# Kernel optimization log

Measured on AMD Instinct MI355X. Metric: run time of the kernel, lower is better.

The kernel has to match this reference:

```python
import jax, jax.numpy as jnp
import numpy as np

NEGPOS_RATIO = 3


def _smooth_l1(pred, tgt):
    d = jnp.abs(pred - tgt)
    return jnp.where(d < 1.0, 0.5 * d * d, d - 0.5)


def setup_inputs() -> dict:
    key = jax.random.key(0)
    B, P, C = 64, 8732, 81
    ks = jax.random.split(key, 7)
    loc_dataT = jax.random.normal(ks[0], (B, P, 4), jnp.float32)
    conf_dataT = jax.random.normal(ks[1], (B, P, C), jnp.float32)
    loc_dataS = jax.random.normal(ks[2], (B, P, 4), jnp.float32)
    conf_dataS = jax.random.normal(ks[3], (B, P, C), jnp.float32)
    loc_t = jax.random.normal(ks[4], (B, P, 4), jnp.float32)
    is_pos = jax.random.uniform(ks[5], (B, P)) < 0.02
    labels = jax.random.randint(ks[6], (B, P), 1, C, dtype=jnp.int32)
    conf_t = jnp.where(is_pos, labels, 0).astype(jnp.int32)
    return {
        "loc_dataT": loc_dataT, "conf_dataT": conf_dataT,
        "loc_dataS": loc_dataS, "conf_dataS": conf_dataS,
        "loc_t": loc_t, "conf_t": conf_t,
    }


def _multibox_losses(loc_dataT, conf_dataT, loc_dataS, conf_dataS, loc_t, conf_t):
    B, P, C = conf_dataT.shape
    pos = conf_t > 0                                    # [B,P]
    posf = pos.astype(conf_dataT.dtype)

    # Localization SmoothL1 over positive priors (reduction='sum')
    loss_lT = jnp.sum(_smooth_l1(loc_dataT, loc_t) * posf[..., None])
    loss_lS = jnp.sum(_smooth_l1(loc_dataS, loc_t) * posf[..., None])

    # Per-prior CE loss: logsumexp(conf) - conf[gt]  (== -log_softmax[gt])
    def per_prior_ce(conf):
        lse = jax.nn.logsumexp(conf, axis=-1)           # [B,P]
        gt = jnp.take_along_axis(conf, conf_t[..., None].astype(jnp.int32), axis=-1)[..., 0]
        return lse - gt

    lcT = per_prior_ce(conf_dataT)                      # [B,P]
    lcS = per_prior_ce(conf_dataS)

    # Hard negative mining: rank negatives by loss (positives zeroed first)
    def neg_mask(lc, num_neg):
        lc_m = jnp.where(pos, 0.0, lc)
        order = jnp.argsort(-lc_m, axis=1)              # descending sort indices
        rank = jnp.argsort(order, axis=1)               # rank of each prior
        return rank < num_neg

    num_pos = jnp.sum(pos.astype(jnp.int32), axis=1, keepdims=True)   # [B,1]
    num_neg = jnp.minimum(NEGPOS_RATIO * num_pos, P - 1)
    negT = neg_mask(lcT, num_neg)
    negS = neg_mask(lcS, num_neg)

    # Confidence CE over positives + mined negatives (reduction='sum')
    loss_cT = jnp.sum(jnp.where(pos | negT, lcT, 0.0))
    loss_cS = jnp.sum(jnp.where(pos | negS, lcS, 0.0))

    N = jnp.sum(num_pos).astype(conf_dataT.dtype)
    return jnp.stack([loss_lT / N, loss_cT / N, loss_lS / N, loss_cS / N])


def reference(loc_dataT, conf_dataT, loc_dataS, conf_dataS, loc_t, conf_t):
    # Teacher branch is detached in the original module.
    loc_dataT = jax.lax.stop_gradient(loc_dataT)
    conf_dataT = jax.lax.stop_gradient(conf_dataT)
    return _multibox_losses(loc_dataT, conf_dataT, loc_dataS, conf_dataS, loc_t, conf_t)
```

## Files before the change

kernel.cpp:

```cpp
#include <hip/hip_runtime.h>

#define BB 64
#define PP 8732
#define CC 81
#define RPW 16
#define WSLOTS ((RPW * CC) / 4)
#define WSTRIDE (WSLOTS + RPW)
#define WPB 4
#define ROWS_PB (RPW * WPB)


__device__ __forceinline__ float sl1(float d) {
    d = fabsf(d);
    return d < 1.0f ? 0.5f * d * d : d - 0.5f;
}

__device__ __forceinline__ float blockReduceF(float v, volatile float* sb) {
    for (int off = 32; off; off >>= 1) v += __shfl_xor(v, off, 64);
    __syncthreads();
    if ((threadIdx.x & 63) == 0) sb[threadIdx.x >> 6] = v;
    __syncthreads();
    float r = 0.0f;
    int nw = blockDim.x >> 6;
    for (int i = 0; i < nw; ++i) r += sb[i];
    return r;
}

__device__ __forceinline__ int blockReduceI(int v, volatile int* sb) {
    for (int off = 32; off; off >>= 1) v += __shfl_xor(v, off, 64);
    __syncthreads();
    if ((threadIdx.x & 63) == 0) sb[threadIdx.x >> 6] = v;
    __syncthreads();
    int r = 0;
    int nw = blockDim.x >> 6;
    for (int i = 0; i < nw; ++i) r += sb[i];
    return r;
}

__global__ void kInit(float* acc, int* numpos, int* ctr, float* locPart) {
    int t = threadIdx.x;
    if (t < 4) acc[t] = 0.0f;
    if (t < BB) { numpos[t] = 0; locPart[t] = 0.0f; locPart[BB + t] = 0.0f; }
    if (t == 0) ctr[0] = 0;
}

__device__ __forceinline__ void processSlot(int i, float4 v,
                                            float* psum, float* spill) {
    int f = i << 2;
    int r0 = f / 81;
    int rem = f - r0 * 81;
    float e0 = __expf(v.x), e1 = __expf(v.y), e2 = __expf(v.z), e3 = __expf(v.w);
    float t01 = e0 + e1;
    float tot = t01 + e2 + e3;
    float ps = tot;
    if (rem >= 78) {
        int ns = 81 - rem;
        float a = (ns == 1) ? e0 : ((ns == 2) ? t01 : t01 + e2);
        ps = a;
        spill[r0 + 1] = tot - a;
    }
    psum[i] = ps;
}

__global__ __launch_bounds__(256, 8) void kStream(
        const float* __restrict__ confT, const float* __restrict__ confS,
        const int* __restrict__ conft,
        const float4* __restrict__ locT4, const float4* __restrict__ locS4,
        const float4* __restrict__ loct4,
        float* __restrict__ lcT, float* __restrict__ lcS,
        float* __restrict__ locPart, int* __restrict__ numpos) {
    __shared__ float lds[WPB * WSTRIDE];
    int b = blockIdx.y;
    int z = blockIdx.z;
    int tid = threadIdx.x;
    int w = tid >> 6, lane = tid & 63;
    int row0 = blockIdx.x * ROWS_PB + w * RPW;
    int nr = min(RPW, PP - row0);
    const float* __restrict__ conf = z ? confS : confT;
    float* __restrict__ dst = z ? lcS : lcT;
    float* psum = lds + w * WSTRIDE;
    float* spill = psum + WSLOTS;

    float sT = 0.0f, sS = 0.0f;
    int cnt = 0;
    int g_ = 0;

    if (nr > 0) {
        size_t rowBase = (size_t)b * PP + row0;
        const float* __restrict__ rowp = conf + rowBase * (size_t)CC;
        const float4* __restrict__ g4 = (const float4*)rowp;
        bool hasrow = lane < nr;
        if (hasrow) g_ = conft[rowBase + lane];
        float gtv = 0.0f;

        if (nr == RPW) {
            float4 v0 = g4[lane];
            float4 v1 = g4[lane + 64];
            float4 v2 = g4[lane + 128];
            float4 v3 = g4[lane + 192];
            float4 v4 = g4[lane + 256];
            float4 vx;
            bool extra = lane < (WSLOTS - 320);
            if (extra) vx = g4[320 + lane];
            if (hasrow) gtv = rowp[lane * CC + g_];
            processSlot(lane,       v0, psum, spill);
            processSlot(lane + 64,  v1, psum, spill);
            processSlot(lane + 128, v2, psum, spill);
            processSlot(lane + 192, v3, psum, spill);
            processSlot(lane + 256, v4, psum, spill);
            if (extra) processSlot(320 + lane, vx, psum, spill);
        } else {
            int nq = (nr * CC) >> 2;
            for (int i = lane; i < nq; i += 64)
                processSlot(i, g4[i], psum, spill);
            if (hasrow) gtv = rowp[lane * CC + g_];
        }

        if (z == 0 && hasrow && g_ > 0) {
            size_t idx = rowBase + lane;
            float4 gt = loct4[idx];
            float4 aT = locT4[idx];
            float4 aS = locS4[idx];
            sT = sl1(aT.x - gt.x) + sl1(aT.y - gt.y) + sl1(aT.z - gt.z) + sl1(aT.w - gt.w);
            sS = sl1(aS.x - gt.x) + sl1(aS.y - gt.y) + sl1(aS.z - gt.z) + sl1(aS.w - gt.w);
            cnt = 1;
        }

        asm volatile("s_waitcnt lgkmcnt(0)" ::: "memory");
        __builtin_amdgcn_sched_barrier(0);

        int r = lane >> 2, h = lane & 3;
        float gv = __shfl(gtv, r, 64);
        int   gr = __shfl(g_,  r, 64);
        if (r < nr) {
            int i0 = (81 * r + 3) >> 2;
            int i1 = (81 * (r + 1) + 3) >> 2;
            float s = (h == 0 && (r & 3)) ? spill[r] : 0.0f;
            for (int i = i0 + h; i < i1; i += 4) s += psum[i];
            s += __shfl_xor(s, 1, 64);
            s += __shfl_xor(s, 2, 64);
            if (h == 0) {
                float lc = __logf(s) - gv;
                dst[rowBase + r] = (gr > 0) ? -(lc + 1.0f) : lc;
            }
        }
    }

    if (z == 0) {
        for (int off = 32; off; off >>= 1) {
            sT  += __shfl_xor(sT,  off, 64);
            sS  += __shfl_xor(sS,  off, 64);
            cnt += __shfl_xor(cnt, off, 64);
        }
        if (lane == 0 && cnt) {
            atomicAdd(&locPart[b], sT);
            atomicAdd(&locPart[BB + b], sS);
            atomicAdd(&numpos[b], cnt);
        }
    }
}

__global__ __launch_bounds__(1024) void kC(const float* __restrict__ lcT,
                                           const float* __restrict__ lcS,
                                           const int* __restrict__ numpos,
                                           const float* __restrict__ locPart,
                                           float* acc, int* ctr,
                                           float* __restrict__ out) {
    __shared__ unsigned keys[PP];
    __shared__ int whist[16 * 256];
    __shared__ int hist[256];
    __shared__ float fsb[16];
    __shared__ int isb[16];
    __shared__ int selBin, selAbove, lastFlag, wsum[4];
    int b = blockIdx.y;
    int tid = threadIdx.x;
    int lane = tid & 63;
    const float* src = ((blockIdx.x == 0) ? lcT : lcS) + (size_t)b * PP;

    float posSum = 0.0f;
    for (int i = tid; i < PP; i += 1024) {
        float v = src[i];
        keys[i] = (v < 0.0f) ? 0u : __float_as_uint(v);
        if (v < 0.0f) posSum += (-v - 1.0f);
    }
    posSum = blockReduceF(posSum, fsb);

    int np = numpos[b];
    int k = min(3 * np, PP - 1);
    float mined = 0.0f;
    if (k > 0) {
        unsigned prefix = 0;
        int kk = k;
        int wid = tid >> 6;
        for (int round = 0; round < 4; ++round) {
            int shift = 24 - 8 * round;
            for (int i = tid; i < 16 * 256; i += 1024) whist[i] = 0;
            __syncthreads();
            for (int i = tid; i < PP; i += 1024) {
                unsigned key = keys[i];
                bool match = (round == 0) || ((key >> (shift + 8)) == prefix);
                if (match) atomicAdd(&whist[(wid << 8) | ((key >> shift) & 0xFF)], 1);
            }
            __syncthreads();
            if (tid < 256) {
                int h2 = 0;
                #pragma unroll
                for (int w = 0; w < 16; ++w) h2 += whist[(w << 8) | tid];
                hist[tid] = h2;
            }
            __syncthreads();
            int x = (tid < 256) ? hist[tid] : 0;
            for (int d = 1; d < 64; d <<= 1) {
                int y = __shfl_down(x, d, 64);
                if (lane + d < 64) x += y;
            }
            if (tid < 256 && lane == 0) wsum[tid >> 6] = x;
            __syncthreads();
            if (tid < 256) {
                int wv = tid >> 6;
                int add = 0;
                if (wv < 3) add += wsum[wv + 1];
                if (wv < 2) add += wsum[wv + 2];
                if (wv < 1) add += wsum[wv + 3];
                int sfx = x + add;
                hist[tid] = sfx;
            }
            __syncthreads();
            if (tid < 256) {
                int above = (tid < 255) ? hist[tid + 1] : 0;
                if (above < kk && hist[tid] >= kk) {
                    selBin = tid;
                    selAbove = above;
                }
            }
            __syncthreads();
            prefix = (prefix << 8) | (unsigned)selBin;
            kk -= selAbove;
            __syncthreads();
        }
        int c = 0;
        float s = 0.0f;
        for (int i = tid; i < PP; i += 1024) {
            unsigned key = keys[i];
            if (key > prefix) { c += 1; s += __uint_as_float(key); }
        }
        c = blockReduceI(c, isb);
        s = blockReduceF(s, fsb);
        mined = s + (float)(k - c) * __uint_as_float(prefix);
    }
    if (tid == 0) {
        atomicAdd(&acc[(blockIdx.x == 0) ? 2 : 3], posSum + mined);
        __threadfence();
        int old = atomicAdd(ctr, 1);
        lastFlag = (old == 2 * BB - 1) ? 1 : 0;
    }
    __syncthreads();
    if (lastFlag) {
        __threadfence();
        int v = 0;
        float pT = 0.0f, pS = 0.0f;
        if (tid < BB) {
            v  = __hip_atomic_load(&numpos[tid], __ATOMIC_RELAXED, __HIP_MEMORY_SCOPE_AGENT);
            pT = __hip_atomic_load(&locPart[tid], __ATOMIC_RELAXED, __HIP_MEMORY_SCOPE_AGENT);
            pS = __hip_atomic_load(&locPart[BB + tid], __ATOMIC_RELAXED, __HIP_MEMORY_SCOPE_AGENT);
        }
        if (tid < 64) {
            for (int off = 32; off; off >>= 1) {
                v  += __shfl_xor(v,  off, 64);
                pT += __shfl_xor(pT, off, 64);
                pS += __shfl_xor(pS, off, 64);
            }
        }
        if (tid == 0) {
            float N = (float)v;
            float a2 = __hip_atomic_load(&acc[2], __ATOMIC_RELAXED, __HIP_MEMORY_SCOPE_AGENT);
            float a3 = __hip_atomic_load(&acc[3], __ATOMIC_RELAXED, __HIP_MEMORY_SCOPE_AGENT);
            out[0] = pT / N;
            out[1] = a2 / N;
            out[2] = pS / N;
            out[3] = a3 / N;
        }
    }
}

extern "C" void kernel_launch(void* const* d_in, const int* in_sizes, int n_in,
                              void* d_out, int out_size, void* d_ws, size_t ws_size,
                              hipStream_t stream) {
    const float* locT  = (const float*)d_in[0];
    const float* confT = (const float*)d_in[1];
    const float* locS  = (const float*)d_in[2];
    const float* confS = (const float*)d_in[3];
    const float* loct  = (const float*)d_in[4];
    const int*   conft = (const int*)d_in[5];
    float* out = (float*)d_out;

    float* lcT = (float*)d_ws;
    float* lcS = lcT + (size_t)BB * PP;
    float* acc = lcS + (size_t)BB * PP;
    int* numpos = (int*)(acc + 4);
    int* ctr = numpos + BB;
    float* locPart = (float*)(ctr + 1);

    kInit<<<1, 64, 0, stream>>>(acc, numpos, ctr, locPart);

    dim3 gS((PP + ROWS_PB - 1) / ROWS_PB, BB, 2);
    kStream<<<gS, 256, 0, stream>>>(confT, confS, conft,
                                    (const float4*)locT, (const float4*)locS,
                                    (const float4*)loct, lcT, lcS,
                                    locPart, numpos);

    dim3 gC(2, BB);
    kC<<<gC, 1024, 0, stream>>>(lcT, lcS, numpos, locPart, acc, ctr, out);
}
```

Measured before the change: 425.4 us.

## Process teacher and student conf rows in the same wave instead of separate grid z

The kernel drops the z grid dimension. Each wave now loads both the teacher and student conf tiles up front, then runs the exp/partial-sum and per-row reduction twice, reusing the same LDS scratch. The goal is to double the memory-level parallelism per wave, share the conft label load, and halve the block count. In exchange, register pressure rises, which the lower launch bound of 6 waves per SIMD accommodates, and occupancy may drop.

```diff
diff --git a/kernel.cpp b/kernel.cpp
--- a/kernel.cpp
+++ b/kernel.cpp
@@ -62,7 +62,29 @@
     psum[i] = ps;
 }
 
-__global__ __launch_bounds__(256, 8) void kStream(
+__device__ __forceinline__ void waveReduceStore(float* __restrict__ dst,
+                                                size_t rowBase, int nr, int lane,
+                                                const float* psum,
+                                                const float* spill,
+                                                float gtv, int g_) {
+    int r = lane >> 2, h = lane & 3;
+    float gv = __shfl(gtv, r, 64);
+    int   gr = __shfl(g_,  r, 64);
+    if (r < nr) {
+        int i0 = (81 * r + 3) >> 2;
+        int i1 = (81 * (r + 1) + 3) >> 2;
+        float s = (h == 0 && (r & 3)) ? spill[r] : 0.0f;
+        for (int i = i0 + h; i < i1; i += 4) s += psum[i];
+        s += __shfl_xor(s, 1, 64);
+        s += __shfl_xor(s, 2, 64);
+        if (h == 0) {
+            float lc = __logf(s) - gv;
+            dst[rowBase + r] = (gr > 0) ? -(lc + 1.0f) : lc;
+        }
+    }
+}
+
+__global__ __launch_bounds__(256, 6) void kStream(
         const float* __restrict__ confT, const float* __restrict__ confS,
         const int* __restrict__ conft,
         const float4* __restrict__ locT4, const float4* __restrict__ locS4,
@@ -71,52 +93,87 @@
         float* __restrict__ locPart, int* __restrict__ numpos) {
     __shared__ float lds[WPB * WSTRIDE];
     int b = blockIdx.y;
-    int z = blockIdx.z;
     int tid = threadIdx.x;
     int w = tid >> 6, lane = tid & 63;
     int row0 = blockIdx.x * ROWS_PB + w * RPW;
     int nr = min(RPW, PP - row0);
-    const float* __restrict__ conf = z ? confS : confT;
-    float* __restrict__ dst = z ? lcS : lcT;
     float* psum = lds + w * WSTRIDE;
     float* spill = psum + WSLOTS;
 
     float sT = 0.0f, sS = 0.0f;
     int cnt = 0;
     int g_ = 0;
+    bool hasrow = false;
 
     if (nr > 0) {
         size_t rowBase = (size_t)b * PP + row0;
-        const float* __restrict__ rowp = conf + rowBase * (size_t)CC;
-        const float4* __restrict__ g4 = (const float4*)rowp;
-        bool hasrow = lane < nr;
-        if (hasrow) g_ = conft[rowBase + lane];
-        float gtv = 0.0f;
+        const float* __restrict__ rowT = confT + rowBase * (size_t)CC;
+        const float* __restrict__ rowS = confS + rowBase * (size_t)CC;
+        const float4* __restrict__ gT4 = (const float4*)rowT;
+        const float4* __restrict__ gS4 = (const float4*)rowS;
+        hasrow = lane < nr;
 
         if (nr == RPW) {
-            float4 v0 = g4[lane];
-            float4 v1 = g4[lane + 64];
-            float4 v2 = g4[lane + 128];
-            float4 v3 = g4[lane + 192];
-            float4 v4 = g4[lane + 256];
-            float4 vx;
+            if (hasrow) g_ = conft[rowBase + lane];
+            float4 t0 = gT4[lane];
+            float4 t1 = gT4[lane + 64];
+            float4 t2 = gT4[lane + 128];
+            float4 t3 = gT4[lane + 192];
+            float4 t4 = gT4[lane + 256];
+            float4 tx;
             bool extra = lane < (WSLOTS - 320);
-            if (extra) vx = g4[320 + lane];
-            if (hasrow) gtv = rowp[lane * CC + g_];
-            processSlot(lane,       v0, psum, spill);
-            processSlot(lane + 64,  v1, psum, spill);
-            processSlot(lane + 128, v2, psum, spill);
-            processSlot(lane + 192, v3, psum, spill);
-            processSlot(lane + 256, v4, psum, spill);
-            if (extra) processSlot(320 + lane, vx, psum, spill);
+            if (extra) tx = gT4[320 + lane];
+            float4 s0 = gS4[lane];
+            float4 s1 = gS4[lane + 64];
+            float4 s2 = gS4[lane + 128];
+            float4 s3 = gS4[lane + 192];
+            float4 s4 = gS4[lane + 256];
+            float4 sx;
+            if (extra) sx = gS4[320 + lane];
+            float gtvT = 0.0f, gtvS = 0.0f;
+            if (hasrow) {
+                gtvT = rowT[lane * CC + g_];
+                gtvS = rowS[lane * CC + g_];
+            }
+            __builtin_amdgcn_sched_barrier(0);
+
+            processSlot(lane,       t0, psum, spill);
+            processSlot(lane + 64,  t1, psum, spill);
+            processSlot(lane + 128, t2, psum, spill);
+            processSlot(lane + 192, t3, psum, spill);
+            processSlot(lane + 256, t4, psum, spill);
+            if (extra) processSlot(320 + lane, tx, psum, spill);
+            asm volatile("s_waitcnt lgkmcnt(0)" ::: "memory");
+            __builtin_amdgcn_sched_barrier(0);
+            waveReduceStore(lcT, rowBase, nr, lane, psum, spill, gtvT, g_);
+
+            processSlot(lane,       s0, psum, spill);
+            processSlot(lane + 64,  s1, psum, spill);
+            processSlot(lane + 128, s2, psum, spill);
+            processSlot(lane + 192, s3, psum, spill);
+            processSlot(lane + 256, s4, psum, spill);
+            if (extra) processSlot(320 + lane, sx, psum, spill);
+            asm volatile("s_waitcnt lgkmcnt(0)" ::: "memory");
+            __builtin_amdgcn_sched_barrier(0);
+            waveReduceStore(lcS, rowBase, nr, lane, psum, spill, gtvS, g_);
         } else {
             int nq = (nr * CC) >> 2;
+            if (hasrow) g_ = conft[rowBase + lane];
             for (int i = lane; i < nq; i += 64)
-                processSlot(i, g4[i], psum, spill);
-            if (hasrow) gtv = rowp[lane * CC + g_];
-        }
-
-        if (z == 0 && hasrow && g_ > 0) {
+                processSlot(i, gT4[i], psum, spill);
+            float gtvT = hasrow ? rowT[lane * CC + g_] : 0.0f;
+            asm volatile("s_waitcnt lgkmcnt(0)" ::: "memory");
+            __builtin_amdgcn_sched_barrier(0);
+            waveReduceStore(lcT, rowBase, nr, lane, psum, spill, gtvT, g_);
+            for (int i = lane; i < nq; i += 64)
+                processSlot(i, gS4[i], psum, spill);
+            float gtvS = hasrow ? rowS[lane * CC + g_] : 0.0f;
+            asm volatile("s_waitcnt lgkmcnt(0)" ::: "memory");
+            __builtin_amdgcn_sched_barrier(0);
+            waveReduceStore(lcS, rowBase, nr, lane, psum, spill, gtvS, g_);
+        }
+
+        if (hasrow && g_ > 0) {
             size_t idx = rowBase + lane;
             float4 gt = loct4[idx];
             float4 aT = locT4[idx];
@@ -125,38 +182,17 @@
             sS = sl1(aS.x - gt.x) + sl1(aS.y - gt.y) + sl1(aS.z - gt.z) + sl1(aS.w - gt.w);
             cnt = 1;
         }
-
-        asm volatile("s_waitcnt lgkmcnt(0)" ::: "memory");
-        __builtin_amdgcn_sched_barrier(0);
-
-        int r = lane >> 2, h = lane & 3;
-        float gv = __shfl(gtv, r, 64);
-        int   gr = __shfl(g_,  r, 64);
-        if (r < nr) {
-            int i0 = (81 * r + 3) >> 2;
-            int i1 = (81 * (r + 1) + 3) >> 2;
-            float s = (h == 0 && (r & 3)) ? spill[r] : 0.0f;
-            for (int i = i0 + h; i < i1; i += 4) s += psum[i];
-            s += __shfl_xor(s, 1, 64);
-            s += __shfl_xor(s, 2, 64);
-            if (h == 0) {
-                float lc = __logf(s) - gv;
-                dst[rowBase + r] = (gr > 0) ? -(lc + 1.0f) : lc;
-            }
-        }
-    }
-
-    if (z == 0) {
-        for (int off = 32; off; off >>= 1) {
-            sT  += __shfl_xor(sT,  off, 64);
-            sS  += __shfl_xor(sS,  off, 64);
-            cnt += __shfl_xor(cnt, off, 64);
-        }
-        if (lane == 0 && cnt) {
-            atomicAdd(&locPart[b], sT);
-            atomicAdd(&locPart[BB + b], sS);
-            atomicAdd(&numpos[b], cnt);
-        }
+    }
+
+    for (int off = 32; off; off >>= 1) {
+        sT  += __shfl_xor(sT,  off, 64);
+        sS  += __shfl_xor(sS,  off, 64);
+        cnt += __shfl_xor(cnt, off, 64);
+    }
+    if (lane == 0 && cnt) {
+        atomicAdd(&locPart[b], sT);
+        atomicAdd(&locPart[BB + b], sS);
+        atomicAdd(&numpos[b], cnt);
     }
 }
 
@@ -303,7 +339,7 @@
 
     kInit<<<1, 64, 0, stream>>>(acc, numpos, ctr, locPart);
 
-    dim3 gS((PP + ROWS_PB - 1) / ROWS_PB, BB, 2);
+    dim3 gS((PP + ROWS_PB - 1) / ROWS_PB, BB);
     kStream<<<gS, 256, 0, stream>>>(confT, confS, conft,
                                     (const float4*)locT, (const float4*)locS,
                                     (const float4*)loct, lcT, lcS,
```

Result: faster. 417.0 us (-2.0%).

## Switch streaming kernel to one-thread-per-row logsumexp and rotate histogram bins

Applied to the files above, without the earlier changes.

The conf streaming kernel drops the wave-cooperative float4 load plus LDS partial-sum scheme. Each thread now handles one prior and reads its whole 81-float row from both teacher and student tensors with aligned float4 loads, so the separate z dimension of the grid goes away. This removes the LDS traffic and the shuffle reduction, but consecutive lanes now read addresses 324 bytes apart, which hurts coalescing and leans on cache lines being reused across lanes. The radix-select histogram also offsets each wave's bins by a per-wave amount, meant to spread its LDS atomics across different banks.

```diff
diff --git a/kernel.cpp b/kernel.cpp
--- a/kernel.cpp
+++ b/kernel.cpp
@@ -3,11 +3,6 @@
 #define BB 64
 #define PP 8732
 #define CC 81
-#define RPW 16
-#define WSLOTS ((RPW * CC) / 4)
-#define WSTRIDE (WSLOTS + RPW)
-#define WPB 4
-#define ROWS_PB (RPW * WPB)
 
 
 __device__ __forceinline__ float sl1(float d) {
@@ -44,22 +39,28 @@
     if (t == 0) ctr[0] = 0;
 }
 
-__device__ __forceinline__ void processSlot(int i, float4 v,
-                                            float* psum, float* spill) {
-    int f = i << 2;
-    int r0 = f / 81;
-    int rem = f - r0 * 81;
-    float e0 = __expf(v.x), e1 = __expf(v.y), e2 = __expf(v.z), e3 = __expf(v.w);
-    float t01 = e0 + e1;
-    float tot = t01 + e2 + e3;
-    float ps = tot;
-    if (rem >= 78) {
-        int ns = 81 - rem;
-        float a = (ns == 1) ? e0 : ((ns == 2) ? t01 : t01 + e2);
-        ps = a;
-        spill[r0 + 1] = tot - a;
-    }
-    psum[i] = ps;
+__device__ __forceinline__ float rowSumExp(const float* __restrict__ conf,
+                                           size_t f0, int d) {
+    const float4* __restrict__ p = (const float4*)(conf + (f0 - (size_t)d));
+    float4 v0 = p[0];
+    float a0 = (d <= 0) ? __expf(v0.x) : 0.0f;
+    float a1 = (d <= 1) ? __expf(v0.y) : 0.0f;
+    float a2 = (d <= 2) ? __expf(v0.z) : 0.0f;
+    float a3 = __expf(v0.w);
+    #pragma unroll
+    for (int k = 1; k < 20; ++k) {
+        float4 v = p[k];
+        a0 += __expf(v.x);
+        a1 += __expf(v.y);
+        a2 += __expf(v.z);
+        a3 += __expf(v.w);
+    }
+    float4 vl = p[20];
+    a0 += __expf(vl.x);
+    a1 += (d >= 1) ? __expf(vl.y) : 0.0f;
+    a2 += (d >= 2) ? __expf(vl.z) : 0.0f;
+    a3 += (d >= 3) ? __expf(vl.w) : 0.0f;
+    return (a0 + a1) + (a2 + a3);
 }
 
 __global__ __launch_bounds__(256, 8) void kStream(
@@ -69,97 +70,54 @@
         const float4* __restrict__ loct4,
         float* __restrict__ lcT, float* __restrict__ lcS,
         float* __restrict__ locPart, int* __restrict__ numpos) {
-    __shared__ float lds[WPB * WSTRIDE];
     int b = blockIdx.y;
-    int z = blockIdx.z;
-    int tid = threadIdx.x;
-    int w = tid >> 6, lane = tid & 63;
-    int row0 = blockIdx.x * ROWS_PB + w * RPW;
-    int nr = min(RPW, PP - row0);
-    const float* __restrict__ conf = z ? confS : confT;
-    float* __restrict__ dst = z ? lcS : lcT;
-    float* psum = lds + w * WSTRIDE;
-    float* spill = psum + WSLOTS;
+    int p = blockIdx.x * 256 + threadIdx.x;
+    int lane = threadIdx.x & 63;
 
     float sT = 0.0f, sS = 0.0f;
     int cnt = 0;
-    int g_ = 0;
-
-    if (nr > 0) {
-        size_t rowBase = (size_t)b * PP + row0;
-        const float* __restrict__ rowp = conf + rowBase * (size_t)CC;
-        const float4* __restrict__ g4 = (const float4*)rowp;
-        bool hasrow = lane < nr;
-        if (hasrow) g_ = conft[rowBase + lane];
-        float gtv = 0.0f;
-
-        if (nr == RPW) {
-            float4 v0 = g4[lane];
-            float4 v1 = g4[lane + 64];
-            float4 v2 = g4[lane + 128];
-            float4 v3 = g4[lane + 192];
-            float4 v4 = g4[lane + 256];
-            float4 vx;
-            bool extra = lane < (WSLOTS - 320);
-            if (extra) vx = g4[320 + lane];
-            if (hasrow) gtv = rowp[lane * CC + g_];
-            processSlot(lane,       v0, psum, spill);
-            processSlot(lane + 64,  v1, psum, spill);
-            processSlot(lane + 128, v2, psum, spill);
-            processSlot(lane + 192, v3, psum, spill);
-            processSlot(lane + 256, v4, psum, spill);
-            if (extra) processSlot(320 + lane, vx, psum, spill);
-        } else {
-            int nq = (nr * CC) >> 2;
-            for (int i = lane; i < nq; i += 64)
-                processSlot(i, g4[i], psum, spill);
-            if (hasrow) gtv = rowp[lane * CC + g_];
-        }
-
-        if (z == 0 && hasrow && g_ > 0) {
-            size_t idx = rowBase + lane;
-            float4 gt = loct4[idx];
-            float4 aT = locT4[idx];
-            float4 aS = locS4[idx];
+
+    if (p < PP) {
+        size_t gr = (size_t)b * PP + p;
+        int g = conft[gr];
+        size_t f0 = gr * (size_t)CC;
+        int d = (int)(f0 & 3);
+
+        float sumT = rowSumExp(confT, f0, d);
+        float sumS = rowSumExp(confS, f0, d);
+
+        float gtT = confT[f0 + (size_t)g];
+        float gtS = confS[f0 + (size_t)g];
+
+        float lcTv = __logf(sumT) - gtT;
+        float lcSv = __logf(sumS) - gtS;
+        bool pos = g > 0;
+        lcT[gr] = pos ? -(lcTv + 1.0f) : lcTv;
+        lcS[gr] = pos ? -(lcSv + 1.0f) : lcSv;
+
+        if (pos) {
+            float4 gt = loct4[gr];
+            float4 aT = locT4[gr];
+            float4 aS = locS4[gr];
             sT = sl1(aT.x - gt.x) + sl1(aT.y - gt.y) + sl1(aT.z - gt.z) + sl1(aT.w - gt.w);
             sS = sl1(aS.x - gt.x) + sl1(aS.y - gt.y) + sl1(aS.z - gt.z) + sl1(aS.w - gt.w);
             cnt = 1;
         }
-
-        asm volatile("s_waitcnt lgkmcnt(0)" ::: "memory");
-        __builtin_amdgcn_sched_barrier(0);
-
-        int r = lane >> 2, h = lane & 3;
-        float gv = __shfl(gtv, r, 64);
-        int   gr = __shfl(g_,  r, 64);
-        if (r < nr) {
-            int i0 = (81 * r + 3) >> 2;
-            int i1 = (81 * (r + 1) + 3) >> 2;
-            float s = (h == 0 && (r & 3)) ? spill[r] : 0.0f;
-            for (int i = i0 + h; i < i1; i += 4) s += psum[i];
-            s += __shfl_xor(s, 1, 64);
-            s += __shfl_xor(s, 2, 64);
-            if (h == 0) {
-                float lc = __logf(s) - gv;
-                dst[rowBase + r] = (gr > 0) ? -(lc + 1.0f) : lc;
-            }
-        }
-    }
-
-    if (z == 0) {
-        for (int off = 32; off; off >>= 1) {
-            sT  += __shfl_xor(sT,  off, 64);
-            sS  += __shfl_xor(sS,  off, 64);
-            cnt += __shfl_xor(cnt, off, 64);
-        }
-        if (lane == 0 && cnt) {
-            atomicAdd(&locPart[b], sT);
-            atomicAdd(&locPart[BB + b], sS);
-            atomicAdd(&numpos[b], cnt);
-        }
-    }
-}
-
+    }
+
+    for (int off = 32; off; off >>= 1) {
+        sT  += __shfl_xor(sT,  off, 64);
+        sS  += __shfl_xor(sS,  off, 64);
+        cnt += __shfl_xor(cnt, off, 64);
+    }
+    if (lane == 0 && cnt) {
+        atomicAdd(&locPart[b], sT);
+        atomicAdd(&locPart[BB + b], sS);
+        atomicAdd(&numpos[b], cnt);
+    }
+}
+
+#define WROT(w, bin) (((w) << 8) | (((bin) + (w) * 17) & 0xFF))
 __global__ __launch_bounds__(1024) void kC(const float* __restrict__ lcT,
                                            const float* __restrict__ lcS,
                                            const int* __restrict__ numpos,
@@ -199,13 +157,13 @@
             for (int i = tid; i < PP; i += 1024) {
                 unsigned key = keys[i];
                 bool match = (round == 0) || ((key >> (shift + 8)) == prefix);
-                if (match) atomicAdd(&whist[(wid << 8) | ((key >> shift) & 0xFF)], 1);
+                if (match) atomicAdd(&whist[WROT(wid, (key >> shift) & 0xFF)], 1);
             }
             __syncthreads();
             if (tid < 256) {
                 int h2 = 0;
                 #pragma unroll
-                for (int w = 0; w < 16; ++w) h2 += whist[(w << 8) | tid];
+                for (int w = 0; w < 16; ++w) h2 += whist[WROT(w, tid)];
                 hist[tid] = h2;
             }
             __syncthreads();
@@ -303,7 +261,7 @@
 
     kInit<<<1, 64, 0, stream>>>(acc, numpos, ctr, locPart);
 
-    dim3 gS((PP + ROWS_PB - 1) / ROWS_PB, BB, 2);
+    dim3 gS((PP + 255) / 256, BB);
     kStream<<<gS, 256, 0, stream>>>(confT, confS, conft,
                                     (const float4*)locT, (const float4*)locS,
                                     (const float4*)loct, lcT, lcS,
```

After: 499.4 us. 1.17x slower.

## Fuse streaming CE and hard-negative mining into one kernel with per-batch last-block election

Applied to the files above, without the earlier changes.

Merges the per-prior CE streaming kernel and the radix-select mining kernel into a single launch. Each block now handles 128 rows with 256 threads. A per-batch atomic counter elects the last finishing block, which then runs the top-k selection for both teacher and student, reading the loss values back from global memory instead of caching keys in LDS. This removes one launch and the idle tail between kernels, and lets mining overlap with streaming on other batches. The cost is that mining runs on only 64 blocks of 256 threads, serially over both branches, with more global rereads per radix round.

```diff
diff --git a/kernel.cpp b/kernel.cpp
--- a/kernel.cpp
+++ b/kernel.cpp
@@ -3,11 +3,9 @@
 #define BB 64
 #define PP 8732
 #define CC 81
-#define RPW 16
-#define WSLOTS ((RPW * CC) / 4)
-#define WSTRIDE (WSLOTS + RPW)
-#define WPB 4
-#define ROWS_PB (RPW * WPB)
+#define RPB 128
+#define SLOTS ((RPB * CC) / 4)
+#define NBX ((PP + RPB - 1) / RPB)
 
 
 __device__ __forceinline__ float sl1(float d) {
@@ -37,11 +35,11 @@
     return r;
 }
 
-__global__ void kInit(float* acc, int* numpos, int* ctr, float* locPart) {
+__global__ void kInit(float* acc, int* numpos, float* locPart, int* ctrB, int* ctrF) {
     int t = threadIdx.x;
     if (t < 4) acc[t] = 0.0f;
-    if (t < BB) { numpos[t] = 0; locPart[t] = 0.0f; locPart[BB + t] = 0.0f; }
-    if (t == 0) ctr[0] = 0;
+    if (t < BB) { numpos[t] = 0; locPart[t] = 0.0f; locPart[BB + t] = 0.0f; ctrB[t] = 0; }
+    if (t == 0) ctrF[0] = 0;
 }
 
 __device__ __forceinline__ void processSlot(int i, float4 v,
@@ -62,201 +60,200 @@
     psum[i] = ps;
 }
 
-__global__ __launch_bounds__(256, 8) void kStream(
+__device__ __forceinline__ void phase2(float* __restrict__ dst, size_t rowBase,
+                                       int nrows, int tid,
+                                       const float* psum, const float* spill,
+                                       const float* gtval, const int* gtraw) {
+    int r = tid >> 1, h = tid & 1;
+    if (r < nrows) {
+        int i0 = (81 * r + 3) >> 2;
+        int i1 = (81 * (r + 1) + 3) >> 2;
+        int mid = (i0 + i1 + 1) >> 1;
+        int lo = h ? mid : i0;
+        int hi = h ? i1 : mid;
+        float s = (h == 0 && (r & 3)) ? spill[r] : 0.0f;
+        for (int i = lo; i < hi; ++i) s += psum[i];
+        s += __shfl_xor(s, 1, 64);
+        if (h == 0) {
+            float lc = __logf(s) - gtval[r];
+            dst[rowBase + r] = (gtraw[r] > 0) ? -(lc + 1.0f) : lc;
+        }
+    }
+}
+
+#define WROT4(w, bin) (((w) << 8) | (((bin) + (w) * 17) & 0xFF))
+
+__global__ __launch_bounds__(256) void kFused(
         const float* __restrict__ confT, const float* __restrict__ confS,
         const int* __restrict__ conft,
         const float4* __restrict__ locT4, const float4* __restrict__ locS4,
         const float4* __restrict__ loct4,
         float* __restrict__ lcT, float* __restrict__ lcS,
-        float* __restrict__ locPart, int* __restrict__ numpos) {
-    __shared__ float lds[WPB * WSTRIDE];
+        float* locPart, int* numpos, float* acc,
+        int* ctrB, int* ctrF, float* __restrict__ out) {
+    __shared__ float psum[SLOTS];
+    __shared__ float spill[RPB];
+    __shared__ float gtval[RPB];
+    __shared__ int gtraw[RPB];
+    __shared__ int whist[4 * 256];
+    __shared__ int histS[256];
+    __shared__ float fsb[4];
+    __shared__ int isb[4];
+    __shared__ int selBin, selAbove, mineFlag, finFlag, wsum[4];
+
     int b = blockIdx.y;
     int z = blockIdx.z;
+    int p0 = blockIdx.x * RPB;
+    int nrows = min(RPB, PP - p0);
     int tid = threadIdx.x;
-    int w = tid >> 6, lane = tid & 63;
-    int row0 = blockIdx.x * ROWS_PB + w * RPW;
-    int nr = min(RPW, PP - row0);
+    int lane = tid & 63;
+    int wid = tid >> 6;
     const float* __restrict__ conf = z ? confS : confT;
     float* __restrict__ dst = z ? lcS : lcT;
-    float* psum = lds + w * WSTRIDE;
-    float* spill = psum + WSLOTS;
+    size_t rowBase = (size_t)b * PP + p0;
+    const float* __restrict__ rowp = conf + rowBase * CC;
+    const float4* __restrict__ g4 = (const float4*)rowp;
+
+    bool hasrow = tid < nrows;
+    int g_ = 0;
+    if (hasrow) g_ = conft[rowBase + tid];
+
+    if (nrows == RPB) {
+        float4 v[10];
+        #pragma unroll
+        for (int k = 0; k < 10; ++k) v[k] = g4[tid + 256 * k];
+        float4 vx;
+        bool extra = tid < (SLOTS - 2560);
+        if (extra) vx = g4[2560 + tid];
+        float gtv = 0.0f;
+        if (hasrow) gtv = rowp[tid * CC + g_];
+        __builtin_amdgcn_sched_barrier(0);
+        #pragma unroll
+        for (int k = 0; k < 10; ++k)
+            processSlot(tid + 256 * k, v[k], psum, spill);
+        if (extra) processSlot(2560 + tid, vx, psum, spill);
+        if (hasrow) { gtraw[tid] = g_; gtval[tid] = gtv; }
+    } else {
+        int nq = (nrows * CC) >> 2;
+        for (int i = tid; i < nq; i += 256)
+            processSlot(i, g4[i], psum, spill);
+        float gtv = hasrow ? rowp[tid * CC + g_] : 0.0f;
+        if (hasrow) { gtraw[tid] = g_; gtval[tid] = gtv; }
+    }
+    __syncthreads();
+    phase2(dst, rowBase, nrows, tid, psum, spill, gtval, gtraw);
 
     float sT = 0.0f, sS = 0.0f;
     int cnt = 0;
-    int g_ = 0;
-
-    if (nr > 0) {
-        size_t rowBase = (size_t)b * PP + row0;
-        const float* __restrict__ rowp = conf + rowBase * (size_t)CC;
-        const float4* __restrict__ g4 = (const float4*)rowp;
-        bool hasrow = lane < nr;
-        if (hasrow) g_ = conft[rowBase + lane];
-        float gtv = 0.0f;
-
-        if (nr == RPW) {
-            float4 v0 = g4[lane];
-            float4 v1 = g4[lane + 64];
-            float4 v2 = g4[lane + 128];
-            float4 v3 = g4[lane + 192];
-            float4 v4 = g4[lane + 256];
-            float4 vx;
-            bool extra = lane < (WSLOTS - 320);
-            if (extra) vx = g4[320 + lane];
-            if (hasrow) gtv = rowp[lane * CC + g_];
-            processSlot(lane,       v0, psum, spill);
-            processSlot(lane + 64,  v1, psum, spill);
-            processSlot(lane + 128, v2, psum, spill);
-            processSlot(lane + 192, v3, psum, spill);
-            processSlot(lane + 256, v4, psum, spill);
-            if (extra) processSlot(320 + lane, vx, psum, spill);
-        } else {
-            int nq = (nr * CC) >> 2;
-            for (int i = lane; i < nq; i += 64)
-                processSlot(i, g4[i], psum, spill);
-            if (hasrow) gtv = rowp[lane * CC + g_];
-        }
-
-        if (z == 0 && hasrow && g_ > 0) {
-            size_t idx = rowBase + lane;
-            float4 gt = loct4[idx];
-            float4 aT = locT4[idx];
-            float4 aS = locS4[idx];
-            sT = sl1(aT.x - gt.x) + sl1(aT.y - gt.y) + sl1(aT.z - gt.z) + sl1(aT.w - gt.w);
-            sS = sl1(aS.x - gt.x) + sl1(aS.y - gt.y) + sl1(aS.z - gt.z) + sl1(aS.w - gt.w);
-            cnt = 1;
-        }
-
-        asm volatile("s_waitcnt lgkmcnt(0)" ::: "memory");
-        __builtin_amdgcn_sched_barrier(0);
-
-        int r = lane >> 2, h = lane & 3;
-        float gv = __shfl(gtv, r, 64);
-        int   gr = __shfl(g_,  r, 64);
-        if (r < nr) {
-            int i0 = (81 * r + 3) >> 2;
-            int i1 = (81 * (r + 1) + 3) >> 2;
-            float s = (h == 0 && (r & 3)) ? spill[r] : 0.0f;
-            for (int i = i0 + h; i < i1; i += 4) s += psum[i];
-            s += __shfl_xor(s, 1, 64);
-            s += __shfl_xor(s, 2, 64);
-            if (h == 0) {
-                float lc = __logf(s) - gv;
-                dst[rowBase + r] = (gr > 0) ? -(lc + 1.0f) : lc;
+    if (z == 0 && hasrow && g_ > 0) {
+        size_t idx = rowBase + tid;
+        float4 gt = loct4[idx];
+        float4 aT = locT4[idx];
+        float4 aS = locS4[idx];
+        sT = sl1(aT.x - gt.x) + sl1(aT.y - gt.y) + sl1(aT.z - gt.z) + sl1(aT.w - gt.w);
+        sS = sl1(aS.x - gt.x) + sl1(aS.y - gt.y) + sl1(aS.z - gt.z) + sl1(aS.w - gt.w);
+        cnt = 1;
+    }
+    for (int off = 32; off; off >>= 1) {
+        sT  += __shfl_xor(sT,  off, 64);
+        sS  += __shfl_xor(sS,  off, 64);
+        cnt += __shfl_xor(cnt, off, 64);
+    }
+    if (lane == 0 && cnt) {
+        atomicAdd(&locPart[b], sT);
+        atomicAdd(&locPart[BB + b], sS);
+        atomicAdd(&numpos[b], cnt);
+    }
+
+    __syncthreads();
+    if (tid == 0) {
+        __threadfence();
+        int old = __hip_atomic_fetch_add(&ctrB[b], 1, __ATOMIC_ACQ_REL,
+                                         __HIP_MEMORY_SCOPE_AGENT);
+        mineFlag = (old == 2 * NBX - 1);
+    }
+    __syncthreads();
+    if (!mineFlag) return;
+
+    int np = __hip_atomic_load(&numpos[b], __ATOMIC_RELAXED, __HIP_MEMORY_SCOPE_AGENT);
+    int k = min(3 * np, PP - 1);
+    for (int zz = 0; zz < 2; ++zz) {
+        const float* __restrict__ src = (zz ? lcS : lcT) + (size_t)b * PP;
+        float posSum = 0.0f;
+        for (int i = tid; i < PP; i += 256) {
+            float v = src[i];
+            if (v < 0.0f) posSum += (-v - 1.0f);
+        }
+        posSum = blockReduceF(posSum, fsb);
+        float mined = 0.0f;
+        if (k > 0) {
+            unsigned prefix = 0;
+            int kk = k;
+            for (int round = 0; round < 4; ++round) {
+                int shift = 24 - 8 * round;
+                whist[tid] = 0; whist[256 + tid] = 0;
+                whist[512 + tid] = 0; whist[768 + tid] = 0;
+                __syncthreads();
+                for (int i = tid; i < PP; i += 256) {
+                    float v = src[i];
+                    unsigned key = (v < 0.0f) ? 0u : __float_as_uint(v);
+                    bool match = (round == 0) || ((key >> (shift + 8)) == prefix);
+                    if (match) atomicAdd(&whist[WROT4(wid, (key >> shift) & 0xFF)], 1);
+                }
+                __syncthreads();
+                int h2 = whist[WROT4(0, tid)] + whist[WROT4(1, tid)]
+                       + whist[WROT4(2, tid)] + whist[WROT4(3, tid)];
+                histS[tid] = h2;
+                __syncthreads();
+                int x = histS[tid];
+                for (int d2 = 1; d2 < 64; d2 <<= 1) {
+                    int y = __shfl_down(x, d2, 64);
+                    if (lane + d2 < 64) x += y;
+                }
+                if (lane == 0) wsum[wid] = x;
+                __syncthreads();
+                {
+                    int add = 0;
+                    if (wid < 3) add += wsum[wid + 1];
+                    if (wid < 2) add += wsum[wid + 2];
+                    if (wid < 1) add += wsum[wid + 3];
+                    histS[tid] = x + add;
+                }
+                __syncthreads();
+                {
+                    int above = (tid < 255) ? histS[tid + 1] : 0;
+                    if (above < kk && histS[tid] >= kk) {
+                        selBin = tid;
+                        selAbove = above;
+                    }
+                }
+                __syncthreads();
+                prefix = (prefix << 8) | (unsigned)selBin;
+                kk -= selAbove;
+                __syncthreads();
             }
-        }
-    }
-
-    if (z == 0) {
-        for (int off = 32; off; off >>= 1) {
-            sT  += __shfl_xor(sT,  off, 64);
-            sS  += __shfl_xor(sS,  off, 64);
-            cnt += __shfl_xor(cnt, off, 64);
-        }
-        if (lane == 0 && cnt) {
-            atomicAdd(&locPart[b], sT);
-            atomicAdd(&locPart[BB + b], sS);
-            atomicAdd(&numpos[b], cnt);
-        }
-    }
-}
-
-__global__ __launch_bounds__(1024) void kC(const float* __restrict__ lcT,
-                                           const float* __restrict__ lcS,
-                                           const int* __restrict__ numpos,
-                                           const float* __restrict__ locPart,
-                                           float* acc, int* ctr,
-                                           float* __restrict__ out) {
-    __shared__ unsigned keys[PP];
-    __shared__ int whist[16 * 256];
-    __shared__ int hist[256];
-    __shared__ float fsb[16];
-    __shared__ int isb[16];
-    __shared__ int selBin, selAbove, lastFlag, wsum[4];
-    int b = blockIdx.y;
-    int tid = threadIdx.x;
-    int lane = tid & 63;
-    const float* src = ((blockIdx.x == 0) ? lcT : lcS) + (size_t)b * PP;
-
-    float posSum = 0.0f;
-    for (int i = tid; i < PP; i += 1024) {
-        float v = src[i];
-        keys[i] = (v < 0.0f) ? 0u : __float_as_uint(v);
-        if (v < 0.0f) posSum += (-v - 1.0f);
-    }
-    posSum = blockReduceF(posSum, fsb);
-
-    int np = numpos[b];
-    int k = min(3 * np, PP - 1);
-    float mined = 0.0f;
-    if (k > 0) {
-        unsigned prefix = 0;
-        int kk = k;
-        int wid = tid >> 6;
-        for (int round = 0; round < 4; ++round) {
-            int shift = 24 - 8 * round;
-            for (int i = tid; i < 16 * 256; i += 1024) whist[i] = 0;
-            __syncthreads();
-            for (int i = tid; i < PP; i += 1024) {
-                unsigned key = keys[i];
-                bool match = (round == 0) || ((key >> (shift + 8)) == prefix);
-                if (match) atomicAdd(&whist[(wid << 8) | ((key >> shift) & 0xFF)], 1);
+            int c = 0;
+            float s = 0.0f;
+            for (int i = tid; i < PP; i += 256) {
+                float v = src[i];
+                unsigned key = (v < 0.0f) ? 0u : __float_as_uint(v);
+                if (key > prefix) { c += 1; s += __uint_as_float(key); }
             }
-            __syncthreads();
-            if (tid < 256) {
-                int h2 = 0;
-                #pragma unroll
-                for (int w = 0; w < 16; ++w) h2 += whist[(w << 8) | tid];
-                hist[tid] = h2;
-            }
-            __syncthreads();
-            int x = (tid < 256) ? hist[tid] : 0;
-            for (int d = 1; d < 64; d <<= 1) {
-                int y = __shfl_down(x, d, 64);
-                if (lane + d < 64) x += y;
-            }
-            if (tid < 256 && lane == 0) wsum[tid >> 6] = x;
-            __syncthreads();
-            if (tid < 256) {
-                int wv = tid >> 6;
-                int add = 0;
-                if (wv < 3) add += wsum[wv + 1];
-                if (wv < 2) add += wsum[wv + 2];
-                if (wv < 1) add += wsum[wv + 3];
-                int sfx = x + add;
-                hist[tid] = sfx;
-            }
-            __syncthreads();
-            if (tid < 256) {
-                int above = (tid < 255) ? hist[tid + 1] : 0;
-                if (above < kk && hist[tid] >= kk) {
-                    selBin = tid;
-                    selAbove = above;
-                }
-            }
-            __syncthreads();
-            prefix = (prefix << 8) | (unsigned)selBin;
-            kk -= selAbove;
-            __syncthreads();
-        }
-        int c = 0;
-        float s = 0.0f;
-        for (int i = tid; i < PP; i += 1024) {
-            unsigned key = keys[i];
-            if (key > prefix) { c += 1; s += __uint_as_float(key); }
-        }
-        c = blockReduceI(c, isb);
-        s = blockReduceF(s, fsb);
-        mined = s + (float)(k - c) * __uint_as_float(prefix);
-    }
+            c = blockReduceI(c, isb);
+            s = blockReduceF(s, fsb);
+            mined = s + (float)(k - c) * __uint_as_float(prefix);
+        }
+        if (tid == 0) atomicAdd(&acc[2 + zz], posSum + mined);
+        __syncthreads();
+    }
+
     if (tid == 0) {
-        atomicAdd(&acc[(blockIdx.x == 0) ? 2 : 3], posSum + mined);
-        __threadfence();
-        int old = atomicAdd(ctr, 1);
-        lastFlag = (old == 2 * BB - 1) ? 1 : 0;
-    }
-    __syncthreads();
-    if (lastFlag) {
-        __threadfence();
+        int old = __hip_atomic_fetch_add(ctrF, 1, __ATOMIC_ACQ_REL,
+                                         __HIP_MEMORY_SCOPE_AGENT);
+        finFlag = (old == BB - 1);
+    }
+    __syncthreads();
+    if (finFlag) {
         int v = 0;
         float pT = 0.0f, pS = 0.0f;
         if (tid < BB) {
@@ -298,17 +295,15 @@
     float* lcS = lcT + (size_t)BB * PP;
     float* acc = lcS + (size_t)BB * PP;
     int* numpos = (int*)(acc + 4);
-    int* ctr = numpos + BB;
-    float* locPart = (float*)(ctr + 1);
-
-    kInit<<<1, 64, 0, stream>>>(acc, numpos, ctr, locPart);
-
-    dim3 gS((PP + ROWS_PB - 1) / ROWS_PB, BB, 2);
-    kStream<<<gS, 256, 0, stream>>>(confT, confS, conft,
-                                    (const float4*)locT, (const float4*)locS,
-                                    (const float4*)loct, lcT, lcS,
-                                    locPart, numpos);
-
-    dim3 gC(2, BB);
-    kC<<<gC, 1024, 0, stream>>>(lcT, lcS, numpos, locPart, acc, ctr, out);
-}
+    float* locPart = (float*)(numpos + BB);
+    int* ctrB = (int*)(locPart + 2 * BB);
+    int* ctrF = ctrB + BB;
+
+    kInit<<<1, 64, 0, stream>>>(acc, numpos, locPart, ctrB, ctrF);
+
+    dim3 gF(NBX, BB, 2);
+    kFused<<<gF, 256, 0, stream>>>(confT, confS, conft,
+                                   (const float4*)locT, (const float4*)locS,
+                                   (const float4*)loct, lcT, lcS,
+                                   locPart, numpos, acc, ctrB, ctrF, out);
+}
```

Result: slower. 1.308 ms (+207.4%).
